# Optimization experiments

Hardware: AMD Instinct MI355X
Metric: run time of the kernel (lower is better)

The kernel has to match this reference:

```python
import jax, jax.numpy as jnp
import numpy as np

EPS = 1e-6


def _hungarian(cost):
    """Min-cost rectangular assignment (Kuhn-Munkres with potentials).
    Returns (row_ind, col_ind) matching min(n, m) pairs, like scipy's
    linear_sum_assignment. Cost matrices here are tiny (<= 7x7)."""
    cost = np.asarray(cost, dtype=np.float64)
    transposed = False
    if cost.shape[0] > cost.shape[1]:
        cost = cost.T
        transposed = True
    n, m = cost.shape
    INF = 1e18
    u = np.zeros(n + 1)
    v = np.zeros(m + 1)
    p = np.zeros(m + 1, dtype=np.int64)   # p[j] = row matched to col j (1-indexed)
    way = np.zeros(m + 1, dtype=np.int64)
    for i in range(1, n + 1):
        p[0] = i
        j0 = 0
        minv = np.full(m + 1, INF)
        used = np.zeros(m + 1, dtype=bool)
        while True:
            used[j0] = True
            i0 = p[j0]
            delta = INF
            j1 = 0
            for j in range(1, m + 1):
                if not used[j]:
                    cur = cost[i0 - 1, j - 1] - u[i0] - v[j]
                    if cur < minv[j]:
                        minv[j] = cur
                        way[j] = j0
                    if minv[j] < delta:
                        delta = minv[j]
                        j1 = j
            for j in range(m + 1):
                if used[j]:
                    u[p[j]] += delta
                    v[j] -= delta
                else:
                    minv[j] -= delta
            j0 = j1
            if p[j0] == 0:
                break
        while j0:
            j1 = way[j0]
            p[j0] = p[j1]
            j0 = j1
    rows, cols = [], []
    for j in range(1, m + 1):
        if p[j] != 0:
            rows.append(p[j] - 1)
            cols.append(j - 1)
    if transposed:
        rows, cols = cols, rows
    order = np.argsort(rows)
    return [rows[k] for k in order], [cols[k] for k in order]


def setup_inputs() -> dict:
    key = jax.random.key(0)
    kp, kg, kn = jax.random.split(key, 3)
    B, S, H, W = 32, 8, 256, 256
    pred_attn = jax.random.uniform(kp, (B, S, H, W), dtype=jnp.float32)  # soft slot attention
    gt_masks = jnp.round(jax.random.uniform(kg, (B, S, H, W), dtype=jnp.float32))  # binary GT
    num_objects = jax.random.randint(kn, (B,), 0, 8, dtype=jnp.int32)
    return {"pred_attn": pred_attn, "gt_masks": gt_masks, "num_objects": num_objects}


def _match(dice_mat, num_objects, num_gt):
    """Host-side Hungarian matching on the (negated) dice similarity matrix."""
    cost = -np.asarray(dice_mat)  # (B, P, G)
    nobj = np.asarray(num_objects)
    bi, pi, gi = [], [], []
    for b in range(cost.shape[0]):
        n = int(min(int(nobj[b]), num_gt))
        if n == 0:
            continue
        r, c = _hungarian(cost[b, :, :n])
        bi += [b] * len(r)
        pi += list(r)
        gi += list(c)
    return np.array(bi, np.int64), np.array(pi, np.int64), np.array(gi, np.int64)


def _losses(pred_attn, gt_masks, bi, pi, gi):
    B, S, H, W = pred_attn.shape
    # background dice loss (slot 0)
    bg_p = pred_attn[:, 0].reshape(B, -1)
    bg_g = gt_masks[:, 0].reshape(B, -1)
    inter = (bg_p * bg_g).sum(-1)
    union = bg_p.sum(-1) + bg_g.sum(-1)
    bg_loss = (1.0 - (2.0 * inter + EPS) / (union + EPS)).mean()
    # pairwise dice over all (pred_slot, gt_slot) fg pairs in one einsum
    fg_p = pred_attn[:, 1:].reshape(B, S - 1, -1)  # (B, P, HW)
    fg_g = gt_masks[:, 1:].reshape(B, S - 1, -1)   # (B, G, HW)
    inter_m = jnp.einsum('bpn,bgn->bpg', fg_p, fg_g)
    union_m = fg_p.sum(-1)[:, :, None] + fg_g.sum(-1)[:, None, :]
    dice_m = (2.0 * inter_m + EPS) / (union_m + EPS)  # (B, P, G)
    if bi.size:
        fg_loss = (1.0 - dice_m[bi, pi, gi]).mean()
    else:
        fg_loss = jnp.float32(0.0)
    return bg_loss, fg_loss, dice_m


def reference(pred_attn, gt_masks, num_objects):
    BG_WEIGHT, FG_WEIGHT = 1.0, 1.0
    B, S, H, W = pred_attn.shape
    # build dice similarity matrix once (vectorized; replaces the double loop)
    _, _, dice_m = _losses(pred_attn, gt_masks,
                           np.array([], np.int64), np.array([], np.int64), np.array([], np.int64))
    bi, pi, gi = _match(jax.lax.stop_gradient(dice_m), num_objects, S - 1)
    bg_loss, fg_loss, _ = _losses(pred_attn, gt_masks, bi, pi, gi)
    return BG_WEIGHT * bg_loss + FG_WEIGHT * fg_loss
```

## Files before the change

### kernel.cpp

```cpp
#include <hip/hip_runtime.h>

#define EPSF 1e-6f

__global__ __launch_bounds__(256) void msl_zero(float* __restrict__ acc, int n) {
  int i = blockIdx.x * blockDim.x + threadIdx.x;
  if (i < n) acc[i] = 0.0f;
}

__global__ __launch_bounds__(256) void msl_accum(const float* __restrict__ pred,
                                                 const float* __restrict__ gt,
                                                 float* __restrict__ acc,
                                                 int HW, int HW4) {
  const int b = blockIdx.y;
  const size_t base = (size_t)b * 8 * (size_t)HW;
  const float* P = pred + base;
  const float* G = gt + base;

  float a_bg = 0.0f;
  float af[7][7];
  float sp[8], sg[8];
#pragma unroll
  for (int p = 0; p < 7; ++p)
#pragma unroll
    for (int g = 0; g < 7; ++g) af[p][g] = 0.0f;
#pragma unroll
  for (int s = 0; s < 8; ++s) { sp[s] = 0.0f; sg[s] = 0.0f; }

  const int stride = blockDim.x * gridDim.x;
  for (int i = blockIdx.x * blockDim.x + threadIdx.x; i < HW4; i += stride) {
    float4 pv[8], gv[8];
#pragma unroll
    for (int s = 0; s < 8; ++s)
      pv[s] = ((const float4*)(P + (size_t)s * HW))[i];
#pragma unroll
    for (int s = 0; s < 8; ++s)
      gv[s] = ((const float4*)(G + (size_t)s * HW))[i];

#pragma unroll
    for (int s = 0; s < 8; ++s) {
      sp[s] += (pv[s].x + pv[s].y) + (pv[s].z + pv[s].w);
      sg[s] += (gv[s].x + gv[s].y) + (gv[s].z + gv[s].w);
    }
    a_bg += pv[0].x * gv[0].x + pv[0].y * gv[0].y +
            pv[0].z * gv[0].z + pv[0].w * gv[0].w;
#pragma unroll
    for (int p = 0; p < 7; ++p)
#pragma unroll
      for (int g = 0; g < 7; ++g)
        af[p][g] += pv[p + 1].x * gv[g + 1].x + pv[p + 1].y * gv[g + 1].y +
                    pv[p + 1].z * gv[g + 1].z + pv[p + 1].w * gv[g + 1].w;
  }

  float v[66];
  v[0] = a_bg;
#pragma unroll
  for (int p = 0; p < 7; ++p)
#pragma unroll
    for (int g = 0; g < 7; ++g) v[1 + p * 7 + g] = af[p][g];
#pragma unroll
  for (int s = 0; s < 8; ++s) { v[50 + s] = sp[s]; v[58 + s] = sg[s]; }

#pragma unroll
  for (int k = 0; k < 66; ++k) {
    float x = v[k];
#pragma unroll
    for (int off = 32; off > 0; off >>= 1) x += __shfl_down(x, off, 64);
    v[k] = x;
  }

  __shared__ float red[4][66];
  const int wave = threadIdx.x >> 6;
  const int lane = threadIdx.x & 63;
  if (lane == 0) {
#pragma unroll
    for (int k = 0; k < 66; ++k) red[wave][k] = v[k];
  }
  __syncthreads();
  if (threadIdx.x < 66) {
    float s = red[0][threadIdx.x] + red[1][threadIdx.x] +
              red[2][threadIdx.x] + red[3][threadIdx.x];
    atomicAdd(&acc[b * 66 + threadIdx.x], s);
  }
}

__global__ __launch_bounds__(1024) void msl_final(const float* __restrict__ acc,
                                                  const int* __restrict__ nobj,
                                                  float* __restrict__ out, int B) {
  __shared__ float dp[32][130];
  __shared__ float dice[32][52];
  __shared__ float r_bg[32];
  __shared__ float r_ds[32];
  __shared__ int   r_n[32];

  const int batch = threadIdx.x >> 5;
  const int lane  = threadIdx.x & 31;
  const bool act  = (batch < B);

  if (act) {
    const float* a = acc + batch * 66;
    for (int k = lane; k < 49; k += 32) {
      int p = k / 7, g = k % 7;
      dice[batch][k] = (2.0f * a[1 + k] + EPSF) / (a[51 + p] + a[59 + g] + EPSF);
    }
    if (lane == 0) {
      float u = a[50] + a[58];
      r_bg[batch] = 1.0f - (2.0f * a[0] + EPSF) / (u + EPSF);
      int n = nobj[batch];
      n = n < 0 ? 0 : (n > 7 ? 7 : n);
      r_n[batch] = n;
      r_ds[batch] = 0.0f;
      dp[batch][0] = 0.0f;
    }
  }
  __syncthreads();
  const int n = act ? r_n[batch] : 0;

  for (int c = 1; c <= 7; ++c) {
    if (act && c <= n) {
      for (int mask = lane; mask < 128; mask += 32) {
        if (__popc(mask) == c) {
          float best = -1e30f;
#pragma unroll
          for (int r = 0; r < 7; ++r) {
            if (mask & (1 << r)) {
              float cand = dp[batch][mask ^ (1 << r)] + dice[batch][r * 7 + (c - 1)];
              best = fmaxf(best, cand);
            }
          }
          dp[batch][mask] = best;
        }
      }
    }
    __syncthreads();
  }

  float best = -1e30f;
  if (act && n > 0) {
    for (int mask = lane; mask < 128; mask += 32)
      if (__popc(mask) == n) best = fmaxf(best, dp[batch][mask]);
  }
#pragma unroll
  for (int off = 16; off > 0; off >>= 1)
    best = fmaxf(best, __shfl_down(best, off, 32));
  if (act && lane == 0 && n > 0) r_ds[batch] = best;
  __syncthreads();

  if (threadIdx.x == 0) {
    float bg = 0.0f, ds = 0.0f;
    int cnt = 0;
    for (int b = 0; b < B; ++b) { bg += r_bg[b]; ds += r_ds[b]; cnt += r_n[b]; }
    float fg = cnt > 0 ? ((float)cnt - ds) / (float)cnt : 0.0f;
    out[0] = bg / (float)B + fg;
  }
}

extern "C" void kernel_launch(void* const* d_in, const int* in_sizes, int n_in,
                              void* d_out, int out_size, void* d_ws, size_t ws_size,
                              hipStream_t stream) {
  const float* pred = (const float*)d_in[0];
  const float* gt   = (const float*)d_in[1];
  const int*   nobj = (const int*)d_in[2];
  float* out = (float*)d_out;

  const int B  = in_sizes[2];
  const int HW = in_sizes[0] / (B * 8);
  const int HW4 = HW / 4;

  float* acc = (float*)d_ws;
  const int accN = B * 66;

  msl_zero<<<dim3((accN + 255) / 256), dim3(256), 0, stream>>>(acc, accN);

  const int blocksPerBatch = 32;
  msl_accum<<<dim3(blocksPerBatch, B), dim3(256), 0, stream>>>(pred, gt, acc, HW, HW4);

  msl_final<<<dim3(1), dim3(32 * B), 0, stream>>>(acc, nobj, out, B);
}
```

Measured before the change: 165.7 us.

## Replace atomics with per-block partials, DPP wave reductions, drop zero kernel

Each block now writes its 66 partial sums to its own workspace row instead of atomically adding into a zeroed accumulator, and the final kernel sums the 32 rows per batch. This removes the separate zeroing kernel launch and the atomic contention. The per-wave shuffle reductions are replaced with DPP row/broadcast ops that leave the result in lane 63, and launch bounds request 4 waves-per-EU occupancy. The cost is a larger workspace and a serial 32-row sum inside the single-block final kernel.

```diff
diff --git a/kernel.cpp b/kernel.cpp
--- a/kernel.cpp
+++ b/kernel.cpp
@@ -2,15 +2,20 @@
 
 #define EPSF 1e-6f
 
-__global__ __launch_bounds__(256) void msl_zero(float* __restrict__ acc, int n) {
-  int i = blockIdx.x * blockDim.x + threadIdx.x;
-  if (i < n) acc[i] = 0.0f;
+__device__ __forceinline__ float wave_sum_to_lane63(float x) {
+  x += __int_as_float(__builtin_amdgcn_update_dpp(0, __float_as_int(x), 0x111, 0xf, 0xf, true));
+  x += __int_as_float(__builtin_amdgcn_update_dpp(0, __float_as_int(x), 0x112, 0xf, 0xf, true));
+  x += __int_as_float(__builtin_amdgcn_update_dpp(0, __float_as_int(x), 0x114, 0xf, 0xf, true));
+  x += __int_as_float(__builtin_amdgcn_update_dpp(0, __float_as_int(x), 0x118, 0xf, 0xf, true));
+  x += __int_as_float(__builtin_amdgcn_update_dpp(0, __float_as_int(x), 0x142, 0xa, 0xf, false));
+  x += __int_as_float(__builtin_amdgcn_update_dpp(0, __float_as_int(x), 0x143, 0xc, 0xf, false));
+  return x;
 }
 
-__global__ __launch_bounds__(256) void msl_accum(const float* __restrict__ pred,
-                                                 const float* __restrict__ gt,
-                                                 float* __restrict__ acc,
-                                                 int HW, int HW4) {
+__global__ __launch_bounds__(256, 4) void msl_accum(const float* __restrict__ pred,
+                                                    const float* __restrict__ gt,
+                                                    float* __restrict__ part,
+                                                    int HW, int HW4) {
   const int b = blockIdx.y;
   const size_t base = (size_t)b * 8 * (size_t)HW;
   const float* P = pred + base;
@@ -60,32 +65,29 @@
 #pragma unroll
   for (int s = 0; s < 8; ++s) { v[50 + s] = sp[s]; v[58 + s] = sg[s]; }
 
-#pragma unroll
-  for (int k = 0; k < 66; ++k) {
-    float x = v[k];
-#pragma unroll
-    for (int off = 32; off > 0; off >>= 1) x += __shfl_down(x, off, 64);
-    v[k] = x;
-  }
-
   __shared__ float red[4][66];
   const int wave = threadIdx.x >> 6;
   const int lane = threadIdx.x & 63;
-  if (lane == 0) {
 #pragma unroll
-    for (int k = 0; k < 66; ++k) red[wave][k] = v[k];
+  for (int k = 0; k < 66; ++k) {
+    float x = wave_sum_to_lane63(v[k]);
+    if (lane == 63) red[wave][k] = x;
   }
   __syncthreads();
+
+  const int row = blockIdx.y * gridDim.x + blockIdx.x;
   if (threadIdx.x < 66) {
     float s = red[0][threadIdx.x] + red[1][threadIdx.x] +
               red[2][threadIdx.x] + red[3][threadIdx.x];
-    atomicAdd(&acc[b * 66 + threadIdx.x], s);
+    part[row * 66 + threadIdx.x] = s;
   }
 }
 
-__global__ __launch_bounds__(1024) void msl_final(const float* __restrict__ acc,
+__global__ __launch_bounds__(1024) void msl_final(const float* __restrict__ part,
                                                   const int* __restrict__ nobj,
-                                                  float* __restrict__ out, int B) {
+                                                  float* __restrict__ out,
+                                                  int B, int RPB) {
+  __shared__ float a[32][68];
   __shared__ float dp[32][130];
   __shared__ float dice[32][52];
   __shared__ float r_bg[32];
@@ -97,14 +99,23 @@
   const bool act  = (batch < B);
 
   if (act) {
-    const float* a = acc + batch * 66;
+    for (int k = lane; k < 66; k += 32) {
+      float s = 0.0f;
+      for (int r = 0; r < RPB; ++r) s += part[(batch * RPB + r) * 66 + k];
+      a[batch][k] = s;
+    }
+  }
+  __syncthreads();
+
+  if (act) {
     for (int k = lane; k < 49; k += 32) {
       int p = k / 7, g = k % 7;
-      dice[batch][k] = (2.0f * a[1 + k] + EPSF) / (a[51 + p] + a[59 + g] + EPSF);
+      dice[batch][k] = (2.0f * a[batch][1 + k] + EPSF) /
+                       (a[batch][51 + p] + a[batch][59 + g] + EPSF);
     }
     if (lane == 0) {
-      float u = a[50] + a[58];
-      r_bg[batch] = 1.0f - (2.0f * a[0] + EPSF) / (u + EPSF);
+      float u = a[batch][50] + a[batch][58];
+      r_bg[batch] = 1.0f - (2.0f * a[batch][0] + EPSF) / (u + EPSF);
       int n = nobj[batch];
       n = n < 0 ? 0 : (n > 7 ? 7 : n);
       r_n[batch] = n;
@@ -166,13 +177,10 @@
   const int HW = in_sizes[0] / (B * 8);
   const int HW4 = HW / 4;
 
-  float* acc = (float*)d_ws;
-  const int accN = B * 66;
-
-  msl_zero<<<dim3((accN + 255) / 256), dim3(256), 0, stream>>>(acc, accN);
+  float* part = (float*)d_ws;
 
   const int blocksPerBatch = 32;
-  msl_accum<<<dim3(blocksPerBatch, B), dim3(256), 0, stream>>>(pred, gt, acc, HW, HW4);
+  msl_accum<<<dim3(blocksPerBatch, B), dim3(256), 0, stream>>>(pred, gt, part, HW, HW4);
 
-  msl_final<<<dim3(1), dim3(32 * B), 0, stream>>>(acc, nobj, out, B);
+  msl_final<<<dim3(1), dim3(32 * B), 0, stream>>>(part, nobj, out, B, blocksPerBatch);
 }
```

New measurement: 205.5 us. +24.0%, slower.
